# Kernel tuning notes

Measured on AMD Instinct MI355X. Metric: run time of the kernel, lower is better.

## Reference

```python
import jax, jax.numpy as jnp
import numpy as np

N, IN_DIM, HID = 8192, 128, 64
LEAKY_SLOPE = 0.2
MASK_VAL = -9e15


def lstm_step(x, W_ih, W_hh, b_ih, b_hh, h0, c0):
    # PyTorch LSTM single time step, gate order i, f, g, o
    gates = x @ W_ih.T + b_ih + h0 @ W_hh.T + b_hh
    i, f, g, o = jnp.split(gates, 4, axis=-1)
    c = jax.nn.sigmoid(f) * c0 + jax.nn.sigmoid(i) * jnp.tanh(g)
    h = jax.nn.sigmoid(o) * jnp.tanh(c)
    return h, c


def setup_inputs() -> dict:
    key = jax.random.key(0)
    ks = jax.random.split(key, 10)
    sc = 0.05
    x = jax.random.normal(ks[0], (N, IN_DIM), jnp.float32)
    adj = jax.random.randint(ks[1], (N, N), 0, 2).astype(jnp.float32)
    fea_W = jax.random.normal(ks[2], (IN_DIM, HID), jnp.float32) * sc
    fea_b = jnp.zeros((HID,), jnp.float32)
    gat_W = jax.random.normal(ks[3], (HID, IN_DIM), jnp.float32) * sc
    gat_a = jax.random.normal(ks[4], (2 * IN_DIM,), jnp.float32) * sc
    enc_W_ih = jax.random.normal(ks[5], (4 * HID, IN_DIM), jnp.float32) * sc
    enc_W_hh = jax.random.normal(ks[6], (4 * HID, HID), jnp.float32) * sc
    enc_b_ih = jnp.zeros((4 * HID,), jnp.float32)
    enc_b_hh = jnp.zeros((4 * HID,), jnp.float32)
    dec_W_ih = jax.random.normal(ks[7], (4 * IN_DIM, HID), jnp.float32) * sc
    dec_W_hh = jax.random.normal(ks[8], (4 * IN_DIM, IN_DIM), jnp.float32) * sc
    dec_b_ih = jnp.zeros((4 * IN_DIM,), jnp.float32)
    dec_b_hh = jnp.zeros((4 * IN_DIM,), jnp.float32)
    return dict(x=x, adj=adj, fea_W=fea_W, fea_b=fea_b, gat_W=gat_W, gat_a=gat_a,
                enc_W_ih=enc_W_ih, enc_W_hh=enc_W_hh, enc_b_ih=enc_b_ih, enc_b_hh=enc_b_hh,
                dec_W_ih=dec_W_ih, dec_W_hh=dec_W_hh, dec_b_ih=dec_b_ih, dec_b_hh=dec_b_hh)


def reference(x, adj, fea_W, fea_b, gat_W, gat_a,
              enc_W_ih, enc_W_hh, enc_b_ih, enc_b_hh,
              dec_W_ih, dec_W_hh, dec_b_ih, dec_b_hh):
    # structure branch: Linear + ReLU then GAT layer
    structure = jax.nn.relu(x @ fea_W + fea_b)            # [N, HID]
    Wh = structure @ gat_W                                # [N, IN_DIM]
    a1, a2 = gat_a[:IN_DIM], gat_a[IN_DIM:]
    e = jax.nn.leaky_relu((Wh @ a1)[:, None] + (Wh @ a2)[None, :], LEAKY_SLOPE)  # [N, N]
    scores = jnp.where(adj > 0, e, MASK_VAL)
    att = jax.nn.softmax(scores, axis=1)
    emb = jax.nn.elu(att @ Wh)                            # [N, IN_DIM]
    # attribute branch: seq_len=1 encoder/decoder LSTM with zero init states
    h0e = jnp.zeros((N, HID), x.dtype)
    h_enc, _ = lstm_step(x, enc_W_ih, enc_W_hh, enc_b_ih, enc_b_hh, h0e, h0e)
    h0d = jnp.zeros((N, IN_DIM), x.dtype)
    att_adj, _ = lstm_step(h_enc, dec_W_ih, dec_W_hh, dec_b_ih, dec_b_hh, h0d, h0d)  # [N, IN_DIM]
    con_adj = emb @ emb.T                                 # [N, N]
    return con_adj, att_adj
```

## Files before the change

### kernel.cpp

```cpp
#include <hip/hip_runtime.h>
#include <hip/hip_bf16.h>

typedef __hip_bfloat16 bf16_t;
typedef short bf16x8 __attribute__((ext_vector_type(8)));
typedef float f32x4 __attribute__((ext_vector_type(4)));

#define NROW 8192
#define LEAKY 0.2f

__device__ __forceinline__ float b2f(bf16_t v){ return __bfloat162float(v); }
__device__ __forceinline__ unsigned short f2b(float f){
  union { bf16_t h; unsigned short u; } cv; cv.h = __float2bfloat16(f); return cv.u;
}
__device__ __forceinline__ float sigf(float v){ return 1.0f / (1.0f + __expf(-v)); }

__global__ void k_probe(const unsigned short* __restrict__ x_raw, int* __restrict__ flag)
{
  const int lane = threadIdx.x;
  int cnt = 0;
  for (int k = lane; k < 512; k += 64){
    const int e = (x_raw[k] >> 7) & 0xff;
    cnt += (e >= 120 && e <= 130) ? 1 : 0;
  }
  #pragma unroll
  for (int s = 1; s < 64; s <<= 1) cnt += __shfl_xor(cnt, s, 64);
  if (lane == 0) flag[0] = (cnt < 384) ? 1 : 0;
}

__global__ __launch_bounds__(256) void k_cvt(
    const void* __restrict__ encW, const void* __restrict__ decW,
    const int* __restrict__ flag,
    unsigned short* __restrict__ encWb, unsigned short* __restrict__ decWb)
{
  const int idx = blockIdx.x*256 + threadIdx.x;
  const int isf32 = flag[0];
  if (idx < 32768){
    float v = isf32 ? ((const float*)encW)[idx] : b2f(((const bf16_t*)encW)[idx]);
    encWb[idx] = f2b(v);
  } else {
    const int j = idx - 32768;
    float v = isf32 ? ((const float*)decW)[j] : b2f(((const bf16_t*)decW)[j]);
    decWb[j] = f2b(v);
  }
}

__global__ __launch_bounds__(256) void k_feamask(
    const void* __restrict__ x, const void* __restrict__ adj,
    const void* __restrict__ fea_W, const void* __restrict__ fea_b,
    const void* __restrict__ gat_W, const void* __restrict__ gat_a,
    const int* __restrict__ flag,
    unsigned short* __restrict__ Whb_p, float* __restrict__ s1, float* __restrict__ s2,
    unsigned short* __restrict__ xb, unsigned char* __restrict__ mask8)
{
  const int r = blockIdx.x, tid = threadIdx.x;
  const int isf32 = flag[0];

  float4 mv0, mv1, mv2, mv3, mv4, mv5, mv6, mv7;
  bf16x8 bv0, bv1, bv2, bv3;
  if (isf32){
    const float4* arow = (const float4*)((const float*)adj + (size_t)r*NROW);
    mv0 = arow[(size_t)tid*2];         mv1 = arow[(size_t)tid*2+1];
    mv2 = arow[(size_t)(tid+256)*2];   mv3 = arow[(size_t)(tid+256)*2+1];
    mv4 = arow[(size_t)(tid+512)*2];   mv5 = arow[(size_t)(tid+512)*2+1];
    mv6 = arow[(size_t)(tid+768)*2];   mv7 = arow[(size_t)(tid+768)*2+1];
  } else {
    const unsigned short* arow = (const unsigned short*)adj + (size_t)r*NROW;
    bv0 = *(const bf16x8*)(arow + (size_t)tid*8);
    bv1 = *(const bf16x8*)(arow + (size_t)(tid+256)*8);
    bv2 = *(const bf16x8*)(arow + (size_t)(tid+512)*8);
    bv3 = *(const bf16x8*)(arow + (size_t)(tid+768)*8);
  }

  if (tid < 64){
    const int l = tid;
    float x0, x1;
    if (isf32){
      const float* xr = (const float*)x + (size_t)r*128;
      x0 = xr[l]; x1 = xr[l+64];
    } else {
      const bf16_t* xr = (const bf16_t*)x + (size_t)r*128;
      x0 = b2f(xr[l]); x1 = b2f(xr[l+64]);
    }
    xb[(size_t)r*128 + l]      = f2b(x0);
    xb[(size_t)r*128 + 64 + l] = f2b(x1);

    float acc = isf32 ? ((const float*)fea_b)[l] : b2f(((const bf16_t*)fea_b)[l]);
    if (isf32){
      const float* W = (const float*)fea_W;
      #pragma unroll
      for (int d=0; d<64; ++d) acc = fmaf(__shfl(x0, d, 64), W[d*64+l], acc);
      #pragma unroll
      for (int d=0; d<64; ++d) acc = fmaf(__shfl(x1, d, 64), W[(d+64)*64+l], acc);
    } else {
      const bf16_t* W = (const bf16_t*)fea_W;
      #pragma unroll
      for (int d=0; d<64; ++d) acc = fmaf(__shfl(x0, d, 64), b2f(W[d*64+l]), acc);
      #pragma unroll
      for (int d=0; d<64; ++d) acc = fmaf(__shfl(x1, d, 64), b2f(W[(d+64)*64+l]), acc);
    }
    const float stv = fmaxf(acc, 0.0f);

    float w0 = 0.f, w1 = 0.f;
    if (isf32){
      const float* W = (const float*)gat_W;
      #pragma unroll
      for (int d=0; d<64; ++d){
        const float sd = __shfl(stv, d, 64);
        w0 = fmaf(sd, W[d*128+l],    w0);
        w1 = fmaf(sd, W[d*128+64+l], w1);
      }
    } else {
      const bf16_t* W = (const bf16_t*)gat_W;
      #pragma unroll
      for (int d=0; d<64; ++d){
        const float sd = __shfl(stv, d, 64);
        w0 = fmaf(sd, b2f(W[d*128+l]),    w0);
        w1 = fmaf(sd, b2f(W[d*128+64+l]), w1);
      }
    }

    const size_t pbase = (size_t)(r >> 3)*1024 + (r & 7);
    Whb_p[pbase + (size_t)l*8]        = f2b(w0);
    Whb_p[pbase + (size_t)(l+64)*8]   = f2b(w1);

    float a10, a11, a20, a21;
    if (isf32){
      const float* A = (const float*)gat_a;
      a10 = A[l]; a11 = A[l+64]; a20 = A[128+l]; a21 = A[192+l];
    } else {
      const bf16_t* A = (const bf16_t*)gat_a;
      a10 = b2f(A[l]); a11 = b2f(A[l+64]); a20 = b2f(A[128+l]); a21 = b2f(A[192+l]);
    }
    float r1 = w0*a10 + w1*a11;
    float r2 = w0*a20 + w1*a21;
    #pragma unroll
    for (int s=1; s<64; s<<=1){ r1 += __shfl_xor(r1, s, 64); r2 += __shfl_xor(r2, s, 64); }
    if (l == 0){ s1[r] = r1; s2[r] = r2; }
  }

  if (isf32){
    const float4 va[8] = { mv0, mv1, mv2, mv3, mv4, mv5, mv6, mv7 };
    #pragma unroll
    for (int k=0;k<4;++k){
      const float4 v0 = va[2*k], v1 = va[2*k+1];
      unsigned int m =
          (unsigned int)(v0.x>0.f)      | ((unsigned int)(v0.y>0.f)<<1) |
          ((unsigned int)(v0.z>0.f)<<2) | ((unsigned int)(v0.w>0.f)<<3) |
          ((unsigned int)(v1.x>0.f)<<4) | ((unsigned int)(v1.y>0.f)<<5) |
          ((unsigned int)(v1.z>0.f)<<6) | ((unsigned int)(v1.w>0.f)<<7);
      mask8[(size_t)r*1024 + tid + k*256] = (unsigned char)m;
    }
  } else {
    const bf16x8 vb[4] = { bv0, bv1, bv2, bv3 };
    #pragma unroll
    for (int k=0;k<4;++k){
      unsigned int m = 0;
      #pragma unroll
      for (int j=0;j<8;++j){
        union { short s; unsigned short u; } cv; cv.s = vb[k][j];
        union { unsigned short u; bf16_t h; } cv2; cv2.u = cv.u;
        m |= ((unsigned int)(b2f(cv2.h) > 0.f)) << j;
      }
      mask8[(size_t)r*1024 + tid + k*256] = (unsigned char)m;
    }
  }
}

__global__ __launch_bounds__(256) void k_enc2(
    const unsigned short* __restrict__ xb, const unsigned short* __restrict__ Wb,
    const void* __restrict__ b_ih, const void* __restrict__ b_hh,
    const int* __restrict__ flag, unsigned short* __restrict__ h_enc_b)
{
  __shared__ float g_lds[32][257];
  const int tid = threadIdx.x, lane = tid & 63, wv = tid >> 6;
  const int quad = lane >> 4, nn = lane & 15;
  const int rowbase = blockIdx.x * 32;
  const int rows_off = (wv & 1) * 16;
  const int col_off  = (wv >> 1) * 128;

  f32x4 acc[8];
  #pragma unroll
  for (int t=0;t<8;++t) acc[t] = (f32x4){0.f,0.f,0.f,0.f};

  #pragma unroll
  for (int ks=0; ks<4; ++ks){
    const int kb = ks*32 + quad*8;
    bf16x8 afrag = *(const bf16x8*)(xb + (size_t)(rowbase + rows_off + nn)*128 + kb);
    #pragma unroll
    for (int t=0;t<8;++t){
      bf16x8 bfrag = *(const bf16x8*)(Wb + (size_t)(col_off + t*16 + nn)*128 + kb);
      acc[t] = __builtin_amdgcn_mfma_f32_16x16x32_bf16(afrag, bfrag, acc[t], 0, 0, 0);
    }
  }
  #pragma unroll
  for (int t=0;t<8;++t)
    #pragma unroll
    for (int r=0;r<4;++r)
      g_lds[rows_off + quad*4 + r][col_off + t*16 + nn] = acc[t][r];
  __syncthreads();

  const int isf32 = flag[0];
  #pragma unroll
  for (int k=0;k<8;++k){
    const int idx = tid + k*256;
    const int r = idx >> 6, hid = idx & 63;
    float bi, bg, bo;
    if (isf32){
      const float* bi1 = (const float*)b_ih; const float* bi2 = (const float*)b_hh;
      bi = bi1[hid]     + bi2[hid];
      bg = bi1[128+hid] + bi2[128+hid];
      bo = bi1[192+hid] + bi2[192+hid];
    } else {
      const bf16_t* bi1 = (const bf16_t*)b_ih; const bf16_t* bi2 = (const bf16_t*)b_hh;
      bi = b2f(bi1[hid])     + b2f(bi2[hid]);
      bg = b2f(bi1[128+hid]) + b2f(bi2[128+hid]);
      bo = b2f(bi1[192+hid]) + b2f(bi2[192+hid]);
    }
    const float gi = g_lds[r][hid]     + bi;
    const float gg = g_lds[r][128+hid] + bg;
    const float go = g_lds[r][192+hid] + bo;
    const float c = tanhf(gg) * sigf(gi);
    const float h = tanhf(c)  * sigf(go);
    h_enc_b[(size_t)(rowbase + r)*64 + hid] = f2b(h);
  }
}

__global__ __launch_bounds__(256) void k_dec2(
    const unsigned short* __restrict__ hb, const unsigned short* __restrict__ Wb,
    const void* __restrict__ b_ih, const void* __restrict__ b_hh,
    const int* __restrict__ flag, void* __restrict__ d_out)
{
  __shared__ float g_lds[16][517];
  const int tid = threadIdx.x, lane = tid & 63, wv = tid >> 6;
  const int quad = lane >> 4, nn = lane & 15;
  const int rowbase = blockIdx.x * 16;
  const int col_off = wv * 128;

  f32x4 acc[8];
  #pragma unroll
  for (int t=0;t<8;++t) acc[t] = (f32x4){0.f,0.f,0.f,0.f};

  #pragma unroll
  for (int ks=0; ks<2; ++ks){
    const int kb = ks*32 + quad*8;
    bf16x8 afrag = *(const bf16x8*)(hb + (size_t)(rowbase + nn)*64 + kb);
    #pragma unroll
    for (int t=0;t<8;++t){
      bf16x8 bfrag = *(const bf16x8*)(Wb + (size_t)(col_off + t*16 + nn)*64 + kb);
      acc[t] = __builtin_amdgcn_mfma_f32_16x16x32_bf16(afrag, bfrag, acc[t], 0, 0, 0);
    }
  }
  #pragma unroll
  for (int t=0;t<8;++t)
    #pragma unroll
    for (int r=0;r<4;++r)
      g_lds[quad*4 + r][col_off + t*16 + nn] = acc[t][r];
  __syncthreads();

  const int isf32 = flag[0];
  #pragma unroll
  for (int k=0;k<8;++k){
    const int idx = tid + k*256;
    const int r = idx >> 7, col = idx & 127;
    float bi, bg, bo;
    if (isf32){
      const float* b1 = (const float*)b_ih; const float* b2 = (const float*)b_hh;
      bi = b1[col]     + b2[col];
      bg = b1[256+col] + b2[256+col];
      bo = b1[384+col] + b2[384+col];
    } else {
      const bf16_t* b1 = (const bf16_t*)b_ih; const bf16_t* b2v = (const bf16_t*)b_hh;
      bi = b2f(b1[col])     + b2f(b2v[col]);
      bg = b2f(b1[256+col]) + b2f(b2v[256+col]);
      bo = b2f(b1[384+col]) + b2f(b2v[384+col]);
    }
    const float gi = g_lds[r][col]     + bi;
    const float gg = g_lds[r][256+col] + bg;
    const float go = g_lds[r][384+col] + bo;
    const float c = tanhf(gg) * sigf(gi);
    const float h = tanhf(c)  * sigf(go);
    const size_t oidx = (size_t)NROW*NROW + (size_t)(rowbase + r)*128 + col;
    if (isf32) ((float*)d_out)[oidx] = h;
    else       ((unsigned short*)d_out)[oidx] = f2b(h);
  }
}

__global__ __launch_bounds__(512) void k_attn(
    const unsigned char* __restrict__ mask8, const unsigned short* __restrict__ Whb_p,
    const float* __restrict__ s1g, const float* __restrict__ s2g,
    unsigned short* __restrict__ emb_p)
{
  __shared__ float C_lds[8][16*128];
  __shared__ float dn_lds[8][16];
  const int tid  = threadIdx.x;
  const int lane = tid & 63;
  const int wv   = tid >> 6;
  const int quad = lane >> 4;
  const int mrow = lane & 15;
  const int rowbase = blockIdx.x * 16;
  const float s1row = s1g[rowbase + mrow];
  const unsigned char* mrow_ptr = mask8 + (size_t)(rowbase + mrow) * 1024;

  f32x4 acc[8];
  #pragma unroll
  for (int t=0;t<8;++t) acc[t] = (f32x4){0.f,0.f,0.f,0.f};
  float dn = 0.f;

  const int jbeg = wv * 1024;
  for (int j0 = jbeg; j0 < jbeg + 1024; j0 += 128){
    uint4 mw = *(const uint4*)(mrow_ptr + (j0 >> 3));
    #pragma unroll
    for (int t4=0; t4<4; ++t4){
      const unsigned int wbits = ((const unsigned int*)&mw)[t4];
      const unsigned int mb = (wbits >> (8*quad)) & 0xffu;
      const int kb = j0 + t4*32 + quad*8;
      float4 s2a = *(const float4*)(s2g + kb);
      float4 s2b = *(const float4*)(s2g + kb + 4);
      const float sv[8] = { s2a.x, s2a.y, s2a.z, s2a.w, s2b.x, s2b.y, s2b.z, s2b.w };
      bf16x8 afrag;
      #pragma unroll
      for (int b=0;b<8;++b){
        float v = s1row + sv[b];
        v = (v > 0.f) ? v : LEAKY * v;
        const float e = __expf(v);
        const float p = (mb & (1u<<b)) ? e : 0.f;
        dn += p;
        afrag[b] = (short)f2b(p);
      }
      const unsigned short* wb = Whb_p + (size_t)(kb >> 3)*1024 + mrow*8;
      #pragma unroll
      for (int t=0;t<8;++t){
        bf16x8 bfrag = *(const bf16x8*)(wb + t*128);
        acc[t] = __builtin_amdgcn_mfma_f32_16x16x32_bf16(afrag, bfrag, acc[t], 0, 0, 0);
      }
    }
  }

  #pragma unroll
  for (int t=0;t<8;++t){
    #pragma unroll
    for (int r=0;r<4;++r)
      C_lds[wv][(quad*4+r)*128 + t*16 + mrow] = acc[t][r];
  }
  dn += __shfl_xor(dn, 16, 64);
  dn += __shfl_xor(dn, 32, 64);
  if (lane < 16) dn_lds[wv][lane] = dn;
  __syncthreads();

  for (int idx = tid; idx < 16*128; idx += 512){
    const int m = idx >> 7;
    const int d = idx & 127;
    float v = C_lds[0][idx] + C_lds[1][idx] + C_lds[2][idx] + C_lds[3][idx]
            + C_lds[4][idx] + C_lds[5][idx] + C_lds[6][idx] + C_lds[7][idx];
    const float den = dn_lds[0][m] + dn_lds[1][m] + dn_lds[2][m] + dn_lds[3][m]
                    + dn_lds[4][m] + dn_lds[5][m] + dn_lds[6][m] + dn_lds[7][m];
    v /= den;
    v = (v > 0.f) ? v : (__expf(v) - 1.f);
    emb_p[(size_t)(d >> 3)*65536 + (size_t)(rowbase + m)*8 + (d & 7)] = f2b(v);
  }
}

__global__ __launch_bounds__(256) void k_out(
    const unsigned short* __restrict__ emb_p, const int* __restrict__ flag,
    void* __restrict__ d_out)
{
  const int tid  = threadIdx.x;
  const int lane = tid & 63, wv = tid >> 6;
  const int quad = lane >> 4, nn = lane & 15;
  const int i0 = blockIdx.y * 128 + wv * 32;
  const int j0 = blockIdx.x * 64;

  f32x4 acc[2][4];
  #pragma unroll
  for (int a=0;a<2;++a)
    #pragma unroll
    for (int b=0;b<4;++b) acc[a][b] = (f32x4){0.f,0.f,0.f,0.f};

  #pragma unroll
  for (int ks=0; ks<4; ++ks){
    const int kb = ks*32 + quad*8;
    const unsigned short* base = emb_p + (size_t)(kb >> 3)*65536;
    bf16x8 a0 = *(const bf16x8*)(base + (size_t)(i0 + nn)*8);
    bf16x8 a1 = *(const bf16x8*)(base + (size_t)(i0 + 16 + nn)*8);
    #pragma unroll
    for (int t=0;t<4;++t){
      bf16x8 b = *(const bf16x8*)(base + (size_t)(j0 + t*16 + nn)*8);
      acc[0][t] = __builtin_amdgcn_mfma_f32_16x16x32_bf16(a0, b, acc[0][t], 0, 0, 0);
      acc[1][t] = __builtin_amdgcn_mfma_f32_16x16x32_bf16(a1, b, acc[1][t], 0, 0, 0);
    }
  }

  const int isf32 = flag[0];
  if (isf32){
    float* out = (float*)d_out;
    #pragma unroll
    for (int mi=0; mi<2; ++mi)
      #pragma unroll
      for (int t=0;t<4;++t)
        #pragma unroll
        for (int r=0;r<4;++r)
          out[(size_t)(i0 + mi*16 + quad*4 + r)*NROW + j0 + t*16 + nn] = acc[mi][t][r];
  } else {
    unsigned short* out = (unsigned short*)d_out;
    #pragma unroll
    for (int mi=0; mi<2; ++mi)
      #pragma unroll
      for (int t=0;t<4;++t)
        #pragma unroll
        for (int r=0;r<4;++r)
          out[(size_t)(i0 + mi*16 + quad*4 + r)*NROW + j0 + t*16 + nn] = f2b(acc[mi][t][r]);
  }
}

extern "C" void kernel_launch(void* const* d_in, const int* in_sizes, int n_in,
                              void* d_out, int out_size, void* d_ws, size_t ws_size,
                              hipStream_t stream)
{
  (void)in_sizes; (void)n_in; (void)out_size; (void)ws_size;
  const void* x        = d_in[0];
  const void* adj      = d_in[1];
  const void* fea_W    = d_in[2];
  const void* fea_b    = d_in[3];
  const void* gat_W    = d_in[4];
  const void* gat_a    = d_in[5];
  const void* enc_W_ih = d_in[6];
  const void* enc_b_ih = d_in[8];
  const void* enc_b_hh = d_in[9];
  const void* dec_W_ih = d_in[10];
  const void* dec_b_ih = d_in[12];
  const void* dec_b_hh = d_in[13];

  char* ws = (char*)d_ws;
  unsigned short* Whb_p   = (unsigned short*)ws;
  unsigned short* emb_p   = (unsigned short*)(ws + (2u<<20));
  unsigned short* xb      = (unsigned short*)(ws + (4u<<20));
  unsigned short* h_enc_b = (unsigned short*)(ws + (6u<<20));
  unsigned char*  mask8   = (unsigned char*) (ws + (7u<<20));
  float* s1    = (float*)(ws + (15u<<20));
  float* s2    = (float*)(ws + (15u<<20) + 32768);
  unsigned short* encWb = (unsigned short*)(ws + (15u<<20) + 65536);
  unsigned short* decWb = (unsigned short*)(ws + (15u<<20) + 65536 + 65536);
  int* flag = (int*)(ws + (15u<<20) + 3*65536);

  k_probe<<<1, 64, 0, stream>>>((const unsigned short*)x, flag);
  k_cvt<<<256, 256, 0, stream>>>(enc_W_ih, dec_W_ih, flag, encWb, decWb);
  k_feamask<<<NROW, 256, 0, stream>>>(x, adj, fea_W, fea_b, gat_W, gat_a, flag,
                                      Whb_p, s1, s2, xb, mask8);
  k_enc2<<<256, 256, 0, stream>>>(xb, encWb, enc_b_ih, enc_b_hh, flag, h_enc_b);
  k_dec2<<<512, 256, 0, stream>>>(h_enc_b, decWb, dec_b_ih, dec_b_hh, flag, d_out);
  k_attn<<<512, 512, 0, stream>>>(mask8, Whb_p, s1, s2, emb_p);
  k_out<<<dim3(128, 64), 256, 0, stream>>>(emb_p, flag, d_out);
}
```

Baseline: 592.2 us.

## Process 32 rows per attention block to reuse Wh B-fragments across two MFMA groups

The attention kernel now computes two 16-row groups per block, sharing each loaded Wh B-fragment and s2 vector between two MFMA accumulator sets. This halves global/L2 traffic for Wh per output row. The cost is twice the accumulator registers (lower occupancy), half as many blocks (256 instead of 512 on a large-CU GPU), and a serialized two-pass LDS reduction with extra barriers.

```diff
diff --git a/kernel.cpp b/kernel.cpp
--- a/kernel.cpp
+++ b/kernel.cpp
@@ -120,8 +120,8 @@
     }
 
     const size_t pbase = (size_t)(r >> 3)*1024 + (r & 7);
-    Whb_p[pbase + (size_t)l*8]        = f2b(w0);
-    Whb_p[pbase + (size_t)(l+64)*8]   = f2b(w1);
+    Whb_p[pbase + (size_t)l*8]      = f2b(w0);
+    Whb_p[pbase + (size_t)(l+64)*8] = f2b(w1);
 
     float a10, a11, a20, a21;
     if (isf32){
@@ -285,78 +285,97 @@
   }
 }
 
-__global__ __launch_bounds__(512) void k_attn(
+__global__ __launch_bounds__(512) void k_attn32(
     const unsigned char* __restrict__ mask8, const unsigned short* __restrict__ Whb_p,
     const float* __restrict__ s1g, const float* __restrict__ s2g,
     unsigned short* __restrict__ emb_p)
 {
   __shared__ float C_lds[8][16*128];
-  __shared__ float dn_lds[8][16];
+  __shared__ float dn_lds[8][32];
   const int tid  = threadIdx.x;
   const int lane = tid & 63;
   const int wv   = tid >> 6;
   const int quad = lane >> 4;
   const int mrow = lane & 15;
-  const int rowbase = blockIdx.x * 16;
-  const float s1row = s1g[rowbase + mrow];
-  const unsigned char* mrow_ptr = mask8 + (size_t)(rowbase + mrow) * 1024;
-
-  f32x4 acc[8];
-  #pragma unroll
-  for (int t=0;t<8;++t) acc[t] = (f32x4){0.f,0.f,0.f,0.f};
-  float dn = 0.f;
+  const int rowbase = blockIdx.x * 32;
+  const float s1r0 = s1g[rowbase + mrow];
+  const float s1r1 = s1g[rowbase + 16 + mrow];
+  const unsigned char* mp0 = mask8 + (size_t)(rowbase + mrow) * 1024;
+  const unsigned char* mp1 = mask8 + (size_t)(rowbase + 16 + mrow) * 1024;
+
+  f32x4 acc[2][8];
+  #pragma unroll
+  for (int g=0;g<2;++g)
+    #pragma unroll
+    for (int t=0;t<8;++t) acc[g][t] = (f32x4){0.f,0.f,0.f,0.f};
+  float dn0 = 0.f, dn1 = 0.f;
 
   const int jbeg = wv * 1024;
   for (int j0 = jbeg; j0 < jbeg + 1024; j0 += 128){
-    uint4 mw = *(const uint4*)(mrow_ptr + (j0 >> 3));
+    uint4 mw0 = *(const uint4*)(mp0 + (j0 >> 3));
+    uint4 mw1 = *(const uint4*)(mp1 + (j0 >> 3));
     #pragma unroll
     for (int t4=0; t4<4; ++t4){
-      const unsigned int wbits = ((const unsigned int*)&mw)[t4];
-      const unsigned int mb = (wbits >> (8*quad)) & 0xffu;
+      const unsigned int mb0 = ((((const unsigned int*)&mw0)[t4]) >> (8*quad)) & 0xffu;
+      const unsigned int mb1 = ((((const unsigned int*)&mw1)[t4]) >> (8*quad)) & 0xffu;
       const int kb = j0 + t4*32 + quad*8;
       float4 s2a = *(const float4*)(s2g + kb);
       float4 s2b = *(const float4*)(s2g + kb + 4);
       const float sv[8] = { s2a.x, s2a.y, s2a.z, s2a.w, s2b.x, s2b.y, s2b.z, s2b.w };
-      bf16x8 afrag;
+      bf16x8 af0, af1;
       #pragma unroll
       for (int b=0;b<8;++b){
-        float v = s1row + sv[b];
-        v = (v > 0.f) ? v : LEAKY * v;
-        const float e = __expf(v);
-        const float p = (mb & (1u<<b)) ? e : 0.f;
-        dn += p;
-        afrag[b] = (short)f2b(p);
+        float v0 = s1r0 + sv[b];
+        v0 = (v0 > 0.f) ? v0 : LEAKY * v0;
+        const float e0 = __expf(v0);
+        const float p0 = (mb0 & (1u<<b)) ? e0 : 0.f;
+        dn0 += p0;
+        af0[b] = (short)f2b(p0);
+        float v1 = s1r1 + sv[b];
+        v1 = (v1 > 0.f) ? v1 : LEAKY * v1;
+        const float e1 = __expf(v1);
+        const float p1 = (mb1 & (1u<<b)) ? e1 : 0.f;
+        dn1 += p1;
+        af1[b] = (short)f2b(p1);
       }
       const unsigned short* wb = Whb_p + (size_t)(kb >> 3)*1024 + mrow*8;
       #pragma unroll
       for (int t=0;t<8;++t){
         bf16x8 bfrag = *(const bf16x8*)(wb + t*128);
-        acc[t] = __builtin_amdgcn_mfma_f32_16x16x32_bf16(afrag, bfrag, acc[t], 0, 0, 0);
+        acc[0][t] = __builtin_amdgcn_mfma_f32_16x16x32_bf16(af0, bfrag, acc[0][t], 0, 0, 0);
+        acc[1][t] = __builtin_amdgcn_mfma_f32_16x16x32_bf16(af1, bfrag, acc[1][t], 0, 0, 0);
       }
     }
   }
 
-  #pragma unroll
-  for (int t=0;t<8;++t){
-    #pragma unroll
-    for (int r=0;r<4;++r)
-      C_lds[wv][(quad*4+r)*128 + t*16 + mrow] = acc[t][r];
-  }
-  dn += __shfl_xor(dn, 16, 64);
-  dn += __shfl_xor(dn, 32, 64);
-  if (lane < 16) dn_lds[wv][lane] = dn;
-  __syncthreads();
-
-  for (int idx = tid; idx < 16*128; idx += 512){
-    const int m = idx >> 7;
-    const int d = idx & 127;
-    float v = C_lds[0][idx] + C_lds[1][idx] + C_lds[2][idx] + C_lds[3][idx]
-            + C_lds[4][idx] + C_lds[5][idx] + C_lds[6][idx] + C_lds[7][idx];
-    const float den = dn_lds[0][m] + dn_lds[1][m] + dn_lds[2][m] + dn_lds[3][m]
-                    + dn_lds[4][m] + dn_lds[5][m] + dn_lds[6][m] + dn_lds[7][m];
-    v /= den;
-    v = (v > 0.f) ? v : (__expf(v) - 1.f);
-    emb_p[(size_t)(d >> 3)*65536 + (size_t)(rowbase + m)*8 + (d & 7)] = f2b(v);
+  dn0 += __shfl_xor(dn0, 16, 64);
+  dn0 += __shfl_xor(dn0, 32, 64);
+  dn1 += __shfl_xor(dn1, 16, 64);
+  dn1 += __shfl_xor(dn1, 32, 64);
+  if (lane < 16){ dn_lds[wv][lane] = dn0; dn_lds[wv][16 + lane] = dn1; }
+
+  #pragma unroll
+  for (int rg=0; rg<2; ++rg){
+    #pragma unroll
+    for (int t=0;t<8;++t){
+      #pragma unroll
+      for (int r=0;r<4;++r)
+        C_lds[wv][(quad*4+r)*128 + t*16 + mrow] = acc[rg][t][r];
+    }
+    __syncthreads();
+    for (int idx = tid; idx < 16*128; idx += 512){
+      const int m = idx >> 7;
+      const int d = idx & 127;
+      float v = C_lds[0][idx] + C_lds[1][idx] + C_lds[2][idx] + C_lds[3][idx]
+              + C_lds[4][idx] + C_lds[5][idx] + C_lds[6][idx] + C_lds[7][idx];
+      const float den = dn_lds[0][rg*16+m] + dn_lds[1][rg*16+m] + dn_lds[2][rg*16+m]
+                      + dn_lds[3][rg*16+m] + dn_lds[4][rg*16+m] + dn_lds[5][rg*16+m]
+                      + dn_lds[6][rg*16+m] + dn_lds[7][rg*16+m];
+      v /= den;
+      v = (v > 0.f) ? v : (__expf(v) - 1.f);
+      emb_p[(size_t)(d >> 3)*65536 + (size_t)(rowbase + rg*16 + m)*8 + (d & 7)] = f2b(v);
+    }
+    __syncthreads();
   }
 }
 
@@ -448,6 +467,6 @@
                                       Whb_p, s1, s2, xb, mask8);
   k_enc2<<<256, 256, 0, stream>>>(xb, encWb, enc_b_ih, enc_b_hh, flag, h_enc_b);
   k_dec2<<<512, 256, 0, stream>>>(h_enc_b, decWb, dec_b_ih, dec_b_hh, flag, d_out);
-  k_attn<<<512, 512, 0, stream>>>(mask8, Whb_p, s1, s2, emb_p);
+  k_attn32<<<256, 512, 0, stream>>>(mask8, Whb_p, s1, s2, emb_p);
   k_out<<<dim3(128, 64), 256, 0, stream>>>(emb_p, flag, d_out);
 }
```

Result: faster. 571.9 us (-3.4%).
